# Kernel optimization log

Hardware: AMD Instinct MI355X
Metric: run time of the kernel (lower is better)

Reference implementation:

```python
import jax, jax.numpy as jnp
import numpy as np

Q_DIM = 1024
K_DIM = 1024
HID = 128
EPS = 1e-5


def setup_inputs() -> dict:
    key = jax.random.key(0)
    ks = jax.random.split(key, 12)
    B, Tq, Tk = 2, 512, 512
    s_q = 1.0 / np.sqrt(Q_DIM)
    s_k = 1.0 / np.sqrt(K_DIM)
    s_h3 = 1.0 / np.sqrt(3 * HID)
    s_h = 1.0 / np.sqrt(HID)
    return {
        "Q": jax.random.normal(ks[0], (B, Tq, Q_DIM), jnp.float32),
        "K": jax.random.normal(ks[1], (B, Tk, K_DIM), jnp.float32),
        "Wq": jax.random.uniform(ks[2], (Q_DIM, HID), jnp.float32, -s_q, s_q),
        "Wk": jax.random.uniform(ks[3], (K_DIM, HID), jnp.float32, -s_k, s_k),
        "ln_g": jnp.ones((3 * HID,), jnp.float32),
        "ln_b": jnp.zeros((3 * HID,), jnp.float32),
        "Wu": jax.random.uniform(ks[4], (3 * HID, HID), jnp.float32, -s_h3, s_h3),
        "bu": jax.random.uniform(ks[5], (HID,), jnp.float32, -s_h3, s_h3),
        "Wv": jax.random.uniform(ks[6], (3 * HID, HID), jnp.float32, -s_h3, s_h3),
        "bv": jax.random.uniform(ks[7], (HID,), jnp.float32, -s_h3, s_h3),
        "Wo": jax.random.uniform(ks[8], (HID, 1), jnp.float32, -s_h, s_h),
        "bo": jax.random.uniform(ks[9], (1,), jnp.float32, -s_h, s_h),
    }


def reference(Q, K, Wq, Wk, ln_g, ln_b, Wu, bu, Wv, bv, Wo, bo):
    B, Tq, _ = Q.shape
    Tk = K.shape[1]
    q = jnp.einsum("bqd,dh->bqh", Q, Wq)              # (B,Tq,H)
    k = jnp.einsum("bkd,dh->bkh", K, Wk)              # (B,Tk,H)
    q_exp = jnp.broadcast_to(q[:, :, None, :], (B, Tq, Tk, HID))
    k_exp = jnp.broadcast_to(k[:, None, :, :], (B, Tq, Tk, HID))
    x = jnp.concatenate([q_exp, k_exp, q_exp * k_exp], axis=-1)  # (B,Tq,Tk,3H)
    mu = jnp.mean(x, axis=-1, keepdims=True)
    var = jnp.mean(jnp.square(x - mu), axis=-1, keepdims=True)
    x = (x - mu) * jax.lax.rsqrt(var + EPS) * ln_g + ln_b
    u = jnp.einsum("bqkc,ch->bqkh", x, Wu) + bu
    v = jnp.einsum("bqkc,ch->bqkh", x, Wv) + bv
    z = u * jax.nn.gelu(v, approximate=False)
    return (jnp.einsum("bqkh,ho->bqko", z, Wo) + bo)[..., 0]  # (B,Tq,Tk)
```

## Files before the change

### kernel.cpp

```cpp
#include <hip/hip_runtime.h>
#include <hip/hip_bf16.h>
#include <math.h>


#define EPSLN 1e-5f

#define WS_QP   0
#define WS_KP   131072
#define WS_PU   262144
#define WS_PV   393216
#define WS_RU   524288
#define WS_RV   655360
#define WS_SQ   786432
#define WS_QQ   787456
#define WS_SK   788480
#define WS_KK   789504
#define WS_GUS  790528
#define WS_GVS  790656
#define WS_CU   790784
#define WS_CV   790912
#define WS_WTU  791040
#define WS_WTV  815616
#define WS_WQT  840192
#define WS_WKT  905728

typedef __attribute__((ext_vector_type(8))) short short8;
typedef __attribute__((ext_vector_type(4))) float f32x4;

__device__ inline unsigned short f2bf(float x) {
    unsigned u = __builtin_bit_cast(unsigned, x);
    unsigned r = u + 0x7fffu + ((u >> 16) & 1u);
    return (unsigned short)(r >> 16);
}
__device__ inline float b2f_lo(unsigned v) { return __builtin_bit_cast(float, v << 16); }
__device__ inline float b2f_hi(unsigned v) { return __builtin_bit_cast(float, v & 0xffff0000u); }
__device__ inline unsigned pack_bf2(float a, float b) {
    __hip_bfloat162 h = __float22bfloat162_rn(make_float2(a, b));
    unsigned r;
    __builtin_memcpy(&r, &h, 4);
    return r;
}
__device__ inline void store8(unsigned short* p, const unsigned short* v) {
    short8 s;
    #pragma unroll
    for (int e = 0; e < 8; ++e) s[e] = (short)v[e];
    *(short8*)p = s;
}
#define GELU_C1 2.3022035f
#define GELU_C2 0.1029431f
__device__ inline float fast_gelu(float v) {
    float ex = __builtin_amdgcn_exp2f(v * fmaf(v * v, GELU_C2, GELU_C1));
    float r  = __builtin_amdgcn_rcpf(ex + 1.f);
    return v - v * r;
}

__global__ __launch_bounds__(256, 2)
void k_prep(const float* __restrict__ Wu, const float* __restrict__ bu,
            const float* __restrict__ Wv, const float* __restrict__ bv,
            const float* __restrict__ g, const float* __restrict__ bln,
            const float* __restrict__ Wo,
            const float* __restrict__ Wq, const float* __restrict__ Wk,
            float* __restrict__ ws) {
    int task = blockIdx.x, t = threadIdx.x;
    if (task < 2) {
        bool isV = task != 0;
        const float* W  = isV ? Wv : Wu;
        const float* bb = isV ? bv : bu;
        float* gout = ws + (isV ? WS_GVS : WS_GUS);
        float* cout = ws + (isV ? WS_CV : WS_CU);
        __shared__ float rg[2][128], rc[2][128];
        int tl = t & 127, g2 = t >> 7;
        float gu = 0.f, cu = 0.f;
        for (int c = g2 * 192; c < g2 * 192 + 192; ++c) {
            float wv_ = W[c * 128 + tl];
            gu += g[c] * wv_;
            cu += bln[c] * wv_;
        }
        rg[g2][tl] = gu; rc[g2][tl] = cu;
        __syncthreads();
        if (t < 128) gout[t] = rg[0][t] + rg[1][t];
        else { int h = t - 128; cout[h] = rc[0][h] + rc[1][h] + bb[h]; }
    } else if (task < 8) {
        int tt = task - 2;
        bool isV = tt >= 3;
        int seg = tt % 3;
        const float* W = isV ? Wv : Wu;
        unsigned short* wt = (unsigned short*)(ws + (isV ? WS_WTV : WS_WTU));
        __shared__ unsigned short tile[128 * 130];
        for (int it = 0; it < 64; ++it) {
            int idx = t + 256 * it;
            int c = idx >> 7, h = idx & 127;
            float s = g[seg * 128 + c] * (isV ? 1.f : Wo[h]);
            tile[c * 130 + h] = f2bf(s * W[(seg * 128 + c) * 128 + h]);
        }
        __syncthreads();
        int h = t >> 1, c0 = (t & 1) * 64;
        for (int cc = 0; cc < 64; cc += 8) {
            unsigned short v[8];
            #pragma unroll
            for (int e = 0; e < 8; ++e) v[e] = tile[(c0 + cc + e) * 130 + h];
            store8(&wt[h * 384 + seg * 128 + c0 + cc], v);
        }
    } else {
        int tt = task - 8;
        const float* W = (tt >> 3) ? Wk : Wq;
        unsigned short* wt = (unsigned short*)(ws + ((tt >> 3) ? WS_WKT : WS_WQT));
        int seg = tt & 7;
        __shared__ unsigned short tile[128 * 130];
        for (int it = 0; it < 64; ++it) {
            int idx = t + 256 * it;
            int c = idx >> 7, h = idx & 127;
            tile[c * 130 + h] = f2bf(W[(size_t)(seg * 128 + c) * 128 + h]);
        }
        __syncthreads();
        int h = t >> 1, c0 = (t & 1) * 64;
        for (int cc = 0; cc < 64; cc += 8) {
            unsigned short v[8];
            #pragma unroll
            for (int e = 0; e < 8; ++e) v[e] = tile[(c0 + cc + e) * 130 + h];
            store8(&wt[h * 1024 + seg * 128 + c0 + cc], v);
        }
    }
}

#define XST 1028
#define QST 132
__global__ __launch_bounds__(256, 2)
void k_proj(const float* __restrict__ Q, const float* __restrict__ K,
            float* __restrict__ ws) {
    int blk = blockIdx.x, t = threadIdx.x;
    bool isK = blk >= 128;
    int r0 = (blk & 127) * 8;
    const float* src = isK ? K : Q;
    const unsigned short* wtin = (const unsigned short*)(ws + (isK ? WS_WKT : WS_WQT));
    float* dst = ws + (isK ? WS_KP : WS_QP);
    int L = t & 63, w = t >> 6;
    int col = L & 15, quad = L >> 4;

    __shared__ unsigned short XLb[16 * XST];
    __shared__ unsigned short qpL[16 * QST];
    __shared__ float sp1[16][4], sp2[16][4];

    {
        int srow = t >> 5;
        int c0 = (t & 31) * 4;
        const float* sp = src + (size_t)(r0 + srow) * 1024;
        #pragma unroll
        for (int g8 = 0; g8 < 8; ++g8) {
            float4 xv = *(const float4*)(sp + g8 * 128 + c0);
            unsigned* xp = (unsigned*)&XLb[srow * XST + g8 * 128 + c0];
            xp[0] = pack_bf2(xv.x, xv.y);
            xp[1] = pack_bf2(xv.z, xv.w);
        }
    }
    __syncthreads();

    f32x4 acc[2];
    acc[0] = (f32x4){0.f, 0.f, 0.f, 0.f};
    acc[1] = (f32x4){0.f, 0.f, 0.f, 0.f};
    #pragma unroll 4
    for (int ks = 0; ks < 32; ++ks) {
        short8 a = *(const short8*)&XLb[col * XST + ks * 32 + quad * 8];
        #pragma unroll
        for (int nt2 = 0; nt2 < 2; ++nt2) {
            int h = w * 32 + nt2 * 16 + col;
            short8 b = *(const short8*)&wtin[(size_t)h * 1024 + ks * 32 + quad * 8];
            acc[nt2] = __builtin_amdgcn_mfma_f32_16x16x32_bf16(a, b, acc[nt2], 0, 0, 0);
        }
    }

    #pragma unroll
    for (int r = 0; r < 4; ++r) {
        int row = quad * 4 + r;
        float s1 = acc[0][r] + acc[1][r];
        float s2 = acc[0][r] * acc[0][r] + acc[1][r] * acc[1][r];
        #pragma unroll
        for (int d = 1; d < 16; d <<= 1) { s1 += __shfl_xor(s1, d); s2 += __shfl_xor(s2, d); }
        if (col == 0) { sp1[row][w] = s1; sp2[row][w] = s2; }
        #pragma unroll
        for (int nt2 = 0; nt2 < 2; ++nt2) {
            int h = w * 32 + nt2 * 16 + col;
            qpL[row * QST + h] = f2bf(acc[nt2][r]);
            if (row < 8) dst[(size_t)(r0 + row) * 128 + h] = acc[nt2][r];
        }
    }
    __syncthreads();
    if (t < 8) {
        ws[(isK ? WS_SK : WS_SQ) + r0 + t] = (sp1[t][0] + sp1[t][1]) + (sp1[t][2] + sp1[t][3]);
        ws[(isK ? WS_KK : WS_QQ) + r0 + t] = (sp2[t][0] + sp2[t][1]) + (sp2[t][2] + sp2[t][3]);
    }

    int uv = w & 1, nhf = w >> 1;
    const unsigned short* wt = (const unsigned short*)(ws + (uv ? WS_WTV : WS_WTU));
    int cb0 = isK ? 128 : 0;
    f32x4 pacc[4];
    #pragma unroll
    for (int nt = 0; nt < 4; ++nt) pacc[nt] = (f32x4){0.f, 0.f, 0.f, 0.f};
    #pragma unroll
    for (int ks = 0; ks < 4; ++ks) {
        short8 a = *(const short8*)&qpL[col * QST + ks * 32 + quad * 8];
        #pragma unroll
        for (int nt = 0; nt < 4; ++nt) {
            int h = nhf * 64 + nt * 16 + col;
            short8 b = *(const short8*)&wt[h * 384 + cb0 + ks * 32 + quad * 8];
            pacc[nt] = __builtin_amdgcn_mfma_f32_16x16x32_bf16(a, b, pacc[nt], 0, 0, 0);
        }
    }
    float* PO = ws + (uv ? (isK ? WS_RV : WS_PV) : (isK ? WS_RU : WS_PU));
    #pragma unroll
    for (int nt = 0; nt < 4; ++nt)
        #pragma unroll
        for (int r = 0; r < 4; ++r) {
            int row = quad * 4 + r;
            if (row < 8)
                PO[(size_t)(r0 + row) * 128 + nhf * 64 + nt * 16 + col] = pacc[nt][r];
        }
}

#define ASTR 152
#define RSTR 132
#define REDS 132
__global__ __launch_bounds__(512, 4)
void k_main(const float* __restrict__ ws, float* __restrict__ out,
            const float* __restrict__ Wo, const float* __restrict__ bo) {
    int blk = blockIdx.x;
    int jt = blk & 15, ig = (blk >> 4) & 63, b = blk >> 10;
    int t = threadIdx.x;
    int L = t & 63, w = t >> 6;
    int col = L & 15, quad = L >> 4;
    int krow0 = b * 512 + jt * 32;
    int jj = t >> 4, cb = (t & 15) * 8;
    int h = w * 16 + col;

    __shared__ unsigned short Alds[32 * ASTR];
    __shared__ unsigned ruvL[32 * RSTR];
    __shared__ float red2[32 * REDS];
    __shared__ float skL[32], kkL[32];
    __shared__ float rsL[32], rsmuL[32];

    float kreg[8];
    {
        const float* kp = ws + WS_KP + (size_t)(krow0 + jj) * 128 + cb;
        #pragma unroll
        for (int e = 0; e < 8; ++e) kreg[e] = kp[e];
        const float* rup = ws + WS_RU + (size_t)(krow0 + jj) * 128 + cb;
        const float* rvp = ws + WS_RV + (size_t)(krow0 + jj) * 128 + cb;
        unsigned pk[8];
        #pragma unroll
        for (int e = 0; e < 8; ++e) pk[e] = pack_bf2(rup[e], rvp[e]);
        unsigned* rr = &ruvL[jj * RSTR + cb];
        *(uint4*)&rr[0] = *(uint4*)&pk[0];
        *(uint4*)&rr[4] = *(uint4*)&pk[4];
    }
    if (t < 32) { skL[t] = ws[WS_SK + krow0 + t]; kkL[t] = ws[WS_KK + krow0 + t]; }

    short8 w3f[2][4];
    {
        const unsigned short* wtu = (const unsigned short*)(ws + WS_WTU);
        const unsigned short* wtv = (const unsigned short*)(ws + WS_WTV);
        #pragma unroll
        for (int ks = 0; ks < 4; ++ks) {
            w3f[0][ks] = *(const short8*)&wtu[h * 384 + 256 + ks * 32 + quad * 8];
            w3f[1][ks] = *(const short8*)&wtv[h * 384 + 256 + ks * 32 + quad * 8];
        }
    }
    float wo  = Wo[h];
    float gusv = ws[WS_GUS + h] * wo;
    float cuv  = ws[WS_CU + h] * wo;
    float gvsv = ws[WS_GVS + h];
    float cvv  = ws[WS_CV + h];
    float bo0 = bo[0];
    int bi0 = b * 512 + ig * 8;

    int bi = bi0;
    float4 qA = *(const float4*)(ws + WS_QP + (size_t)bi * 128 + cb);
    float4 qB = *(const float4*)(ws + WS_QP + (size_t)bi * 128 + cb + 4);
    float sqv = ws[WS_SQ + bi];
    float qqv = ws[WS_QQ + bi];
    float puv = ws[WS_PU + (size_t)bi * 128 + h];
    float pvv = ws[WS_PV + (size_t)bi * 128 + h];
    __syncthreads();

    #pragma unroll 1
    for (int ii = 0; ii < 8; ++ii) {
        {
            unsigned pk[4];
            float x0 = kreg[0] * qA.x, x1 = kreg[1] * qA.y;
            float x2 = kreg[2] * qA.z, x3 = kreg[3] * qA.w;
            float y0 = kreg[4] * qB.x, y1 = kreg[5] * qB.y;
            float y2 = kreg[6] * qB.z, y3 = kreg[7] * qB.w;
            float d1 = ((x0 + x1) + (x2 + x3)) + ((y0 + y1) + (y2 + y3));
            float d2 = ((x0 * x0 + x1 * x1) + (x2 * x2 + x3 * x3))
                     + ((y0 * y0 + y1 * y1) + (y2 * y2 + y3 * y3));
            pk[0] = pack_bf2(x0, x1); pk[1] = pack_bf2(x2, x3);
            pk[2] = pack_bf2(y0, y1); pk[3] = pack_bf2(y2, y3);
            unsigned* arow = (unsigned*)Alds + jj * (ASTR / 2) + cb / 2;
            *(uint4*)&arow[0] = *(uint4*)&pk[0];
            d1 += __shfl_xor(d1, 1); d2 += __shfl_xor(d2, 1);
            d1 += __shfl_xor(d1, 2); d2 += __shfl_xor(d2, 2);
            d1 += __shfl_xor(d1, 4); d2 += __shfl_xor(d2, 4);
            d1 += __shfl_xor(d1, 8); d2 += __shfl_xor(d2, 8);
            if ((t & 15) == 0) {
                float mu = (sqv + skL[jj] + d1) * (1.0f / 384.0f);
                float e2 = (qqv + kkL[jj] + d2) * (1.0f / 384.0f);
                float rs = rsqrtf(e2 - mu * mu + EPSLN);
                rsL[jj] = rs;
                rsmuL[jj] = rs * mu;
            }
        }
        int bin = bi0 + ((ii + 1) & 7);
        float4 qA2 = *(const float4*)(ws + WS_QP + (size_t)bin * 128 + cb);
        float4 qB2 = *(const float4*)(ws + WS_QP + (size_t)bin * 128 + cb + 4);
        float sq2 = ws[WS_SQ + bin];
        float qq2 = ws[WS_QQ + bin];
        float pu2 = ws[WS_PU + (size_t)bin * 128 + h];
        float pv2 = ws[WS_PV + (size_t)bin * 128 + h];
        __syncthreads();
        f32x4 acc[2][2];
        #pragma unroll
        for (int mt = 0; mt < 2; ++mt)
            #pragma unroll
            for (int uv = 0; uv < 2; ++uv) acc[mt][uv] = (f32x4){0.f, 0.f, 0.f, 0.f};
        #pragma unroll
        for (int ks = 0; ks < 4; ++ks) {
            short8 a0 = *(const short8*)&Alds[col * ASTR + ks * 32 + quad * 8];
            short8 a1 = *(const short8*)&Alds[(col + 16) * ASTR + ks * 32 + quad * 8];
            acc[0][0] = __builtin_amdgcn_mfma_f32_16x16x32_bf16(a0, w3f[0][ks], acc[0][0], 0, 0, 0);
            acc[0][1] = __builtin_amdgcn_mfma_f32_16x16x32_bf16(a0, w3f[1][ks], acc[0][1], 0, 0, 0);
            acc[1][0] = __builtin_amdgcn_mfma_f32_16x16x32_bf16(a1, w3f[0][ks], acc[1][0], 0, 0, 0);
            acc[1][1] = __builtin_amdgcn_mfma_f32_16x16x32_bf16(a1, w3f[1][ks], acc[1][1], 0, 0, 0);
        }
        #pragma unroll
        for (int mt = 0; mt < 2; ++mt) {
            #pragma unroll
            for (int r = 0; r < 4; ++r) {
                int jl = mt * 16 + quad * 4 + r;
                float rs = rsL[jl];
                float rsmu = rsmuL[jl];
                unsigned pr = ruvL[jl * RSTR + h];
                float su  = acc[mt][0][r] + puv + b2f_lo(pr);
                float u   = fmaf(rs, su, fmaf(-rsmu, gusv, cuv));
                float sv_ = acc[mt][1][r] + pvv + b2f_hi(pr);
                float v   = fmaf(rs, sv_, fmaf(-rsmu, gvsv, cvv));
                red2[jl * REDS + w * 16 + col] = u * fast_gelu(v);
            }
        }
        __syncthreads();
        if (t < 128) {
            const float4* rr = (const float4*)&red2[(t >> 2) * REDS];
            int k = t & 3;
            float s = 0.f;
            #pragma unroll
            for (int c4 = 0; c4 < 8; ++c4) {
                float4 x = rr[k + c4 * 4];
                s += (x.x + x.y) + (x.z + x.w);
            }
            s += __shfl_xor(s, 1);
            s += __shfl_xor(s, 2);
            if (k == 0)
                out[(size_t)bi * 512 + jt * 32 + (t >> 2)] = s + bo0;
        }
        qA = qA2; qB = qB2; sqv = sq2; qqv = qq2; puv = pu2; pvv = pv2; bi = bin;
    }
}

extern "C" void kernel_launch(void* const* d_in, const int* in_sizes, int n_in,
                              void* d_out, int out_size, void* d_ws, size_t ws_size,
                              hipStream_t stream) {
    const float* Q   = (const float*)d_in[0];
    const float* K   = (const float*)d_in[1];
    const float* Wq  = (const float*)d_in[2];
    const float* Wk  = (const float*)d_in[3];
    const float* g   = (const float*)d_in[4];
    const float* bln = (const float*)d_in[5];
    const float* Wu  = (const float*)d_in[6];
    const float* bu  = (const float*)d_in[7];
    const float* Wv  = (const float*)d_in[8];
    const float* bv  = (const float*)d_in[9];
    const float* Wo  = (const float*)d_in[10];
    const float* bo  = (const float*)d_in[11];
    float* ws  = (float*)d_ws;
    float* out = (float*)d_out;

    hipLaunchKernelGGL(k_prep, dim3(24), dim3(256), 0, stream, Wu, bu, Wv, bv, g, bln, Wo, Wq, Wk, ws);
    hipLaunchKernelGGL(k_proj, dim3(256), dim3(256), 0, stream, Q, K, ws);
    hipLaunchKernelGGL(k_main, dim3(2048), dim3(512), 0, stream, ws, out, Wo, bo);
}
```

Measured before the change: 201.1 us.

## Precompute LayerNorm statistics via MFMA and double query rows per block

The per-pair LayerNorm sums (q·k and q²·k²) were computed with shuffle reductions inside every iteration. They are now computed up front for all 16×32 pairs with bf16 MFMA dot products over staged Q, Q², K and K² tiles, and cached in LDS. Each block now handles 16 query rows instead of 8, which halves the grid and amortizes the K/weight setup. Shared memory is aliased into one buffer. Computing the mean and variance terms in bf16 instead of fp32 risks accuracy loss, since variance is taken as E[x²]−mu².

```diff
diff --git a/kernel.cpp b/kernel.cpp
--- a/kernel.cpp
+++ b/kernel.cpp
@@ -71,6 +71,7 @@
         __shared__ float rg[2][128], rc[2][128];
         int tl = t & 127, g2 = t >> 7;
         float gu = 0.f, cu = 0.f;
+        #pragma unroll 4
         for (int c = g2 * 192; c < g2 * 192 + 192; ++c) {
             float wv_ = W[c * 128 + tl];
             gu += g[c] * wv_;
@@ -220,11 +221,12 @@
 #define ASTR 152
 #define RSTR 132
 #define REDS 132
+#define PST  136
 __global__ __launch_bounds__(512, 4)
 void k_main(const float* __restrict__ ws, float* __restrict__ out,
             const float* __restrict__ Wo, const float* __restrict__ bo) {
     int blk = blockIdx.x;
-    int jt = blk & 15, ig = (blk >> 4) & 63, b = blk >> 10;
+    int jt = blk & 15, ig = (blk >> 4) & 31, b = blk >> 9;
     int t = threadIdx.x;
     int L = t & 63, w = t >> 6;
     int col = L & 15, quad = L >> 4;
@@ -232,11 +234,17 @@
     int jj = t >> 4, cb = (t & 15) * 8;
     int h = w * 16 + col;
 
-    __shared__ unsigned short Alds[32 * ASTR];
-    __shared__ unsigned ruvL[32 * RSTR];
-    __shared__ float red2[32 * REDS];
-    __shared__ float skL[32], kkL[32];
-    __shared__ float rsL[32], rsmuL[32];
+    __shared__ __align__(16) char smem[47616];
+    unsigned short* Alds = (unsigned short*)smem;
+    float*          red2 = (float*)(smem + 9728);
+    unsigned short* QL   = (unsigned short*)smem;
+    unsigned short* Q2L  = (unsigned short*)(smem + 4352);
+    unsigned short* KL   = (unsigned short*)(smem + 8704);
+    unsigned short* K2L  = (unsigned short*)(smem + 17408);
+    unsigned*       ruvL = (unsigned*)(smem + 26624);
+    float*          rsL2 = (float*)(smem + 43520);
+
+    int bi0 = b * 512 + ig * 16;
 
     float kreg[8];
     {
@@ -251,8 +259,25 @@
         unsigned* rr = &ruvL[jj * RSTR + cb];
         *(uint4*)&rr[0] = *(uint4*)&pk[0];
         *(uint4*)&rr[4] = *(uint4*)&pk[4];
-    }
-    if (t < 32) { skL[t] = ws[WS_SK + krow0 + t]; kkL[t] = ws[WS_KK + krow0 + t]; }
+        unsigned kk4[4], k2[4];
+        #pragma unroll
+        for (int e = 0; e < 4; ++e) {
+            kk4[e] = pack_bf2(kreg[e * 2], kreg[e * 2 + 1]);
+            k2[e]  = pack_bf2(kreg[e * 2] * kreg[e * 2], kreg[e * 2 + 1] * kreg[e * 2 + 1]);
+        }
+        *(uint4*)&KL[jj * PST + cb]  = *(uint4*)&kk4[0];
+        *(uint4*)&K2L[jj * PST + cb] = *(uint4*)&k2[0];
+    }
+    {
+        int row = t >> 5, c0 = (t & 31) * 4;
+        float4 qv = *(const float4*)(ws + WS_QP + (size_t)(bi0 + row) * 128 + c0);
+        unsigned q01 = pack_bf2(qv.x, qv.y), q23 = pack_bf2(qv.z, qv.w);
+        unsigned s01 = pack_bf2(qv.x * qv.x, qv.y * qv.y);
+        unsigned s23 = pack_bf2(qv.z * qv.z, qv.w * qv.w);
+        uint2 qp = make_uint2(q01, q23), sp = make_uint2(s01, s23);
+        *(uint2*)&QL[row * PST + c0]  = qp;
+        *(uint2*)&Q2L[row * PST + c0] = sp;
+    }
 
     short8 w3f[2][4];
     {
@@ -270,49 +295,56 @@
     float gvsv = ws[WS_GVS + h];
     float cvv  = ws[WS_CV + h];
     float bo0 = bo[0];
-    int bi0 = b * 512 + ig * 8;
 
     int bi = bi0;
     float4 qA = *(const float4*)(ws + WS_QP + (size_t)bi * 128 + cb);
     float4 qB = *(const float4*)(ws + WS_QP + (size_t)bi * 128 + cb + 4);
-    float sqv = ws[WS_SQ + bi];
-    float qqv = ws[WS_QQ + bi];
     float puv = ws[WS_PU + (size_t)bi * 128 + h];
     float pvv = ws[WS_PV + (size_t)bi * 128 + h];
     __syncthreads();
 
+    if (w < 2) {
+        int j = w * 16 + col;
+        f32x4 d1a = (f32x4){0.f, 0.f, 0.f, 0.f};
+        f32x4 d2a = (f32x4){0.f, 0.f, 0.f, 0.f};
+        #pragma unroll
+        for (int ks = 0; ks < 4; ++ks) {
+            short8 aq  = *(const short8*)&QL[col * PST + ks * 32 + quad * 8];
+            short8 bk  = *(const short8*)&KL[j * PST + ks * 32 + quad * 8];
+            d1a = __builtin_amdgcn_mfma_f32_16x16x32_bf16(aq, bk, d1a, 0, 0, 0);
+            short8 aq2 = *(const short8*)&Q2L[col * PST + ks * 32 + quad * 8];
+            short8 bk2 = *(const short8*)&K2L[j * PST + ks * 32 + quad * 8];
+            d2a = __builtin_amdgcn_mfma_f32_16x16x32_bf16(aq2, bk2, d2a, 0, 0, 0);
+        }
+        float skj = ws[WS_SK + krow0 + j];
+        float kkj = ws[WS_KK + krow0 + j];
+        #pragma unroll
+        for (int r = 0; r < 4; ++r) {
+            int i = quad * 4 + r;
+            float mu = (ws[WS_SQ + bi0 + i] + skj + d1a[r]) * (1.0f / 384.0f);
+            float e2 = (ws[WS_QQ + bi0 + i] + kkj + d2a[r]) * (1.0f / 384.0f);
+            float rs = rsqrtf(e2 - mu * mu + EPSLN);
+            *(float2*)&rsL2[(i * 32 + j) * 2] = make_float2(rs, rs * mu);
+        }
+    }
+    __syncthreads();
+
     #pragma unroll 1
-    for (int ii = 0; ii < 8; ++ii) {
+    for (int ii = 0; ii < 16; ++ii) {
         {
             unsigned pk[4];
             float x0 = kreg[0] * qA.x, x1 = kreg[1] * qA.y;
             float x2 = kreg[2] * qA.z, x3 = kreg[3] * qA.w;
             float y0 = kreg[4] * qB.x, y1 = kreg[5] * qB.y;
             float y2 = kreg[6] * qB.z, y3 = kreg[7] * qB.w;
-            float d1 = ((x0 + x1) + (x2 + x3)) + ((y0 + y1) + (y2 + y3));
-            float d2 = ((x0 * x0 + x1 * x1) + (x2 * x2 + x3 * x3))
-                     + ((y0 * y0 + y1 * y1) + (y2 * y2 + y3 * y3));
             pk[0] = pack_bf2(x0, x1); pk[1] = pack_bf2(x2, x3);
             pk[2] = pack_bf2(y0, y1); pk[3] = pack_bf2(y2, y3);
             unsigned* arow = (unsigned*)Alds + jj * (ASTR / 2) + cb / 2;
             *(uint4*)&arow[0] = *(uint4*)&pk[0];
-            d1 += __shfl_xor(d1, 1); d2 += __shfl_xor(d2, 1);
-            d1 += __shfl_xor(d1, 2); d2 += __shfl_xor(d2, 2);
-            d1 += __shfl_xor(d1, 4); d2 += __shfl_xor(d2, 4);
-            d1 += __shfl_xor(d1, 8); d2 += __shfl_xor(d2, 8);
-            if ((t & 15) == 0) {
-                float mu = (sqv + skL[jj] + d1) * (1.0f / 384.0f);
-                float e2 = (qqv + kkL[jj] + d2) * (1.0f / 384.0f);
-                float rs = rsqrtf(e2 - mu * mu + EPSLN);
-                rsL[jj] = rs;
-                rsmuL[jj] = rs * mu;
-            }
-        }
-        int bin = bi0 + ((ii + 1) & 7);
+        }
+        int bin = bi0 + ((ii + 1) & 15);
         float4 qA2 = *(const float4*)(ws + WS_QP + (size_t)bin * 128 + cb);
         float4 qB2 = *(const float4*)(ws + WS_QP + (size_t)bin * 128 + cb + 4);
-        float sq2 = ws[WS_SQ + bin];
-        float qq2 = ws[WS_QQ + bin];
         float pu2 = ws[WS_PU + (size_t)bin * 128 + h];
         float pv2 = ws[WS_PV + (size_t)bin * 128 + h];
         __syncthreads();
@@ -335,8 +367,8 @@
             #pragma unroll
             for (int r = 0; r < 4; ++r) {
                 int jl = mt * 16 + quad * 4 + r;
-                float rs = rsL[jl];
-                float rsmu = rsmuL[jl];
+                float2 rp = *(const float2*)&rsL2[(ii * 32 + jl) * 2];
+                float rs = rp.x, rsmu = rp.y;
                 unsigned pr = ruvL[jl * RSTR + h];
                 float su  = acc[mt][0][r] + puv + b2f_lo(pr);
                 float u   = fmaf(rs, su, fmaf(-rsmu, gusv, cuv));
@@ -360,7 +392,7 @@
             if (k == 0)
                 out[(size_t)bi * 512 + jt * 32 + (t >> 2)] = s + bo0;
         }
-        qA = qA2; qB = qB2; sqv = sq2; qqv = qq2; puv = pu2; pvv = pv2; bi = bin;
+        qA = qA2; qB = qB2; puv = pu2; pvv = pv2; bi = bin;
     }
 }
 
@@ -384,5 +416,5 @@
 
     hipLaunchKernelGGL(k_prep, dim3(24), dim3(256), 0, stream, Wu, bu, Wv, bv, g, bln, Wo, Wq, Wk, ws);
     hipLaunchKernelGGL(k_proj, dim3(256), dim3(256), 0, stream, Q, K, ws);
-    hipLaunchKernelGGL(k_main, dim3(2048), dim3(512), 0, stream, ws, out, Wo, bo);
-}
+    hipLaunchKernelGGL(k_main, dim3(1024), dim3(512), 0, stream, ws, out, Wo, bo);
+}
```

After: 192.7 us. -4.2%, faster.
